# Kernel tuning notes

Measured on AMD Instinct MI355X. Metric: run time of the kernel, lower is better.

The kernel has to match this reference:

```python
import jax, jax.numpy as jnp
import numpy as np

B, S, D, L = 8, 512, 768, 200


def leaky(x, slope=0.2):
    return jnp.where(x >= 0, x, slope * x)


def l1_normalize(x, axis):
    # torch.nn.functional.normalize(p=1): x / max(sum|x|, 1e-12)
    return x / jnp.maximum(jnp.sum(jnp.abs(x), axis=axis, keepdims=True), 1e-12)


def setup_inputs() -> dict:
    key = jax.random.key(0)
    ks = jax.random.split(key, 16)
    s = 1.0 / np.sqrt(D)
    return {
        "doc_embedding": jax.random.normal(ks[0], (B, S, D), jnp.float32),
        "labels": jax.random.uniform(ks[1], (B, L), jnp.float32),
        "label_embed": jax.random.normal(ks[2], (L, D), jnp.float32),
        "label_adj": jax.random.uniform(ks[3], (L, L), jnp.float32),
        "w_gcn3": jax.random.uniform(ks[4], (D, D), jnp.float32, -s, s),
        "w_gcn5": jax.random.uniform(ks[5], (D, D), jnp.float32, -s, s),
        "w_ll1": jax.random.normal(ks[6], (D, D), jnp.float32) * s,
        "b_ll1": jax.random.normal(ks[7], (D,), jnp.float32) * s,
        "w_ll2": jax.random.normal(ks[8], (D, D), jnp.float32) * s,
        "b_ll2": jax.random.normal(ks[9], (D,), jnp.float32) * s,
        "w_lin": jax.random.normal(ks[10], (2 * D, D), jnp.float32) * (1.0 / np.sqrt(2 * D)),
        "b_lin": jax.random.normal(ks[11], (D,), jnp.float32) * s,
        "conv_w": jax.random.normal(ks[12], (L, 1, 9, 9), jnp.float32) * (1.0 / 9.0),
        "conv_b": jax.random.normal(ks[13], (L,), jnp.float32) * 0.01,
        "w_lin1": jax.random.normal(ks[14], (D, L), jnp.float32) * s,
        "b_lin1": jax.random.normal(ks[15], (L,), jnp.float32) * s,
    }


def reference(doc_embedding, labels, label_embed, label_adj, w_gcn3, w_gcn5,
              w_ll1, b_ll1, w_ll2, b_ll2, w_lin, b_lin, conv_w, conv_b,
              w_lin1, b_lin1):
    b = doc_embedding.shape[0]
    # stacked (replicated) label embeddings: [B, L, D]
    le = jnp.broadcast_to(label_embed, (b,) + label_embed.shape)

    # GCN3: adj @ (x @ W), leaky relu 0.2
    le = leaky(jnp.einsum('lm,bmd->bld', label_adj, le @ w_gcn3))

    # learned adjacency A = sigmoid(lin1(le) @ lin2(le)^T)   [B, L, L]
    q = le @ w_ll1 + b_ll1
    k = le @ w_ll2 + b_ll2
    A = jax.nn.sigmoid(jnp.einsum('bld,bmd->blm', q, k))

    # normalize_adj: D^{-1/2} with detached row sum; out = (A D)^T D
    row_sum = jax.lax.stop_gradient(jnp.sum(A, axis=1))  # [B, L]
    d_inv_sqrt = jnp.where(row_sum > 0, row_sum ** -0.5, 0.0)
    AD = A * d_inv_sqrt[:, None, :]                 # A @ diag(d)
    A_norm = jnp.swapaxes(AD, 1, 2) * d_inv_sqrt[:, None, :]

    # GCN5 with learned adj
    d_le = leaky(jnp.einsum('blm,bmd->bld', A_norm, le @ w_gcn5))

    le_cat = jnp.concatenate([le, d_le], axis=-1)   # [B, L, 2D]
    le_out = le_cat @ w_lin + b_lin                 # [B, L, D]

    le_out = l1_normalize(le_out, axis=-2)
    doc = l1_normalize(doc_embedding, axis=-2)

    # word-label attention map [B, S, L]
    wla = jnp.einsum('bsd,bld->bsl', doc, le_out)

    # conv2d 1 -> L channels, 9x9, pad 4 over [B, 1, S, L]
    att = jax.lax.conv_general_dilated(
        wla[:, None, :, :], conv_w, window_strides=(1, 1),
        padding=((4, 4), (4, 4)),
        dimension_numbers=('NCHW', 'OIHW', 'NCHW'))
    att = att + conv_b[None, :, None, None]         # [B, L, S, L]

    att = jnp.max(att, axis=1)                      # [B, S, L]
    att = jnp.max(att, axis=-1, keepdims=True)      # [B, S, 1]
    gate = jnp.tanh(att)

    h_enc = jnp.sum(gate * doc, axis=1)             # [B, D]
    label_output = jax.nn.sigmoid(h_enc @ w_lin1 + b_lin1)

    eps = 1e-7
    p = jnp.clip(label_output, eps, 1.0 - eps)
    loss = -jnp.mean(labels * jnp.log(p) + (1.0 - labels) * jnp.log(1.0 - p))
    return label_output, loss
```

## Files before the change

### kernel.cpp

```cpp
#include <hip/hip_runtime.h>
#include <hip/hip_bf16.h>
#include <math.h>

#define BB 8
#define SS 512
#define DD 768
#define LL 200

typedef __attribute__((ext_vector_type(8))) short bf16x8;
typedef __attribute__((ext_vector_type(4))) float f32x4;

__device__ inline short f2bf(float f) {
    unsigned u = __builtin_bit_cast(unsigned, f);
    unsigned r = (u + 0x7FFFu + ((u >> 16) & 1u)) >> 16;
    return (short)r;
}
__device__ inline float bf2f(short s) {
    unsigned u = ((unsigned)(unsigned short)s) << 16;
    return __builtin_bit_cast(float, u);
}

#define LDP3 264
#define BK3  256
#define MGLDS (2 * 64 * LDP3 * 2)

template<int EPI, bool TB>
__global__ __launch_bounds__(256, 1) void mgemm_k(
    const short* __restrict__ A, int lda,
    const void* __restrict__ Bv, int ldb,
    const float* __restrict__ bias,
    const void* __restrict__ Bv2, const float* __restrict__ bias2, int nsplit,
    const void* __restrict__ Bv3, const float* __restrict__ bias3, int nsplit2,
    float* __restrict__ Cf, int ldc,
    short* __restrict__ Cb, int ldcb,
    short* __restrict__ Ct, int ldct, int nsplitT,
    int M, int N, int K)
{
    extern __shared__ short dsm[];
    short* As = dsm;
    short* Bs = dsm + 64 * LDP3;
    const int tid = threadIdx.x;
    const int bm = blockIdx.y * 64;
    const int bn = blockIdx.x * 64;
    int bnb = bn;
    if (!TB) {
        if (bn >= nsplit2)      { Bv = Bv3; bias = bias3; bnb = bn - nsplit2; }
        else if (bn >= nsplit)  { Bv = Bv2; bias = bias2; bnb = bn - nsplit; }
    }
    const int w = tid >> 6, lane = tid & 63, g = lane >> 4, ln = lane & 15;
    const int Kp = (K + BK3 - 1) & ~(BK3 - 1);
    const int nt = Kp >> 8;

    const int ar = tid >> 2, ac = tid & 3;
    const int bn_ = tid & 63, bko = (tid >> 6) * 64;

    f32x4 acc[4];
    #pragma unroll
    for (int i = 0; i < 4; ++i) acc[i] = (f32x4){0.f, 0.f, 0.f, 0.f};

    bf16x8 aR[8], bT[8];
    #pragma unroll
    for (int j = 0; j < 8; ++j) { aR[j] = (bf16x8){0,0,0,0,0,0,0,0}; bT[j] = (bf16x8){0,0,0,0,0,0,0,0}; }
    float bF[64];
    #pragma unroll
    for (int j = 0; j < 64; ++j) bF[j] = 0.f;

    const int gmS = bm + ar;
    const bool aOk = (gmS < M);

    auto fetchA = [&](int k0) {
        if (aOk) {
            const short* p = A + (size_t)gmS * lda + k0 + ac * 64;
            #pragma unroll
            for (int j = 0; j < 8; ++j) aR[j] = *(const bf16x8*)(p + j * 8);
        }
    };
    auto fetchB = [&](int k0) {
        if (TB) {
            const short* Bt = (const short*)Bv;
            int gn = bn + ar;
            if (gn < N) {
                const short* p = Bt + (size_t)gn * ldb + k0 + ac * 64;
                #pragma unroll
                for (int j = 0; j < 8; ++j) bT[j] = *(const bf16x8*)(p + j * 8);
            }
        } else {
            const float* Bp = (const float*)Bv + (size_t)(bnb + bn_);
            #pragma unroll
            for (int j = 0; j < 64; ++j) {
                int gk = k0 + bko + j;
                bF[j] = (gk < K) ? Bp[(size_t)gk * ldb] : 0.f;
            }
        }
    };

    fetchA(0);
    fetchB(0);

    for (int t = 0; t < nt; ++t) {
        {
            short* pa = As + ar * LDP3 + ac * 64;
            #pragma unroll
            for (int j = 0; j < 8; ++j) *(bf16x8*)(pa + j * 8) = aR[j];
        }
        if (TB) {
            short* pb = Bs + ar * LDP3 + ac * 64;
            #pragma unroll
            for (int j = 0; j < 8; ++j) *(bf16x8*)(pb + j * 8) = bT[j];
        } else {
            short* pb = Bs + bn_ * LDP3 + bko;
            #pragma unroll
            for (int q = 0; q < 8; ++q) {
                bf16x8 v;
                #pragma unroll
                for (int e = 0; e < 8; ++e) v[e] = f2bf(bF[q * 8 + e]);
                *(bf16x8*)(pb + q * 8) = v;
            }
        }
        __syncthreads();

        if (t + 1 < nt) {
            int k0 = (t + 1) << 8;
            fetchA(k0);
            fetchB(k0);
        }

        #pragma unroll
        for (int ks = 0; ks < 8; ++ks) {
            bf16x8 a = *(const bf16x8*)(As + (w * 16 + ln) * LDP3 + ks * 32 + g * 8);
            #pragma unroll
            for (int nb = 0; nb < 4; ++nb) {
                bf16x8 b = *(const bf16x8*)(Bs + (nb * 16 + ln) * LDP3 + ks * 32 + g * 8);
                acc[nb] = __builtin_amdgcn_mfma_f32_16x16x32_bf16(a, b, acc[nb], 0, 0, 0);
            }
        }
        __syncthreads();
    }

    #pragma unroll
    for (int nb = 0; nb < 4; ++nb) {
        int gn = bn + nb * 16 + ln;
        float bv = (bias && gn < N) ? bias[bnb + nb * 16 + ln] : 0.f;
        #pragma unroll
        for (int r = 0; r < 4; ++r) {
            int gm = bm + w * 16 + g * 4 + r;
            if (gm < M && gn < N) {
                float v = acc[nb][r] + bv;
                if (EPI == 1) v = (v >= 0.f) ? v : 0.2f * v;
                else if (EPI == 2) v = 1.f / (1.f + expf(-v));
                if (Cf) Cf[(size_t)gm * ldc + gn] = v;
                if (Cb) Cb[(size_t)gm * ldcb + gn] = f2bf(v);
                if (Ct && gn >= nsplitT)
                    Ct[(size_t)(gn - nsplitT) * ldct + gm] = f2bf(v);
            }
        }
    }
}

#define WP 168
#define TP 24
#define WTR 217
#define WROWS 208
#define APAD 256
#define BIGN (1 << 30)

__global__ void prep_k(const float* __restrict__ cw, const float* __restrict__ cb,
                       const float* __restrict__ adj,
                       short* __restrict__ wkg, short* __restrict__ adj_bf)
{
    int idx = blockIdx.x * blockDim.x + threadIdx.x;
    if (idx < WROWS * WP) {
        int o = idx / WP, kk = idx % WP;
        int kj = kk >> 4, ki = kk & 15;
        float v = 0.f;
        if (o < LL && kj < 9) {
            if (ki < 9) v = cw[o * 81 + ki * 9 + kj];
            else if (ki == 9 && kj == 0) v = cb[o];
        }
        wkg[idx] = f2bf(v);
        return;
    }
    idx -= WROWS * WP;
    if (idx < LL * APAD) {
        int r = idx / APAD, c = idx % APAD;
        adj_bf[idx] = f2bf(c < LL ? adj[r * LL + c] : 0.f);
    }
}

__global__ void ca_k(const float* __restrict__ A, short* __restrict__ An)
{
    int i = blockIdx.x;
    int j = threadIdx.x;
    float si = 0.f, sj = 0.f;
    for (int l = 0; l < LL; ++l) {
        si += A[l * LL + i];
        if (j < LL) sj += A[l * LL + j];
    }
    float di = (si > 0.f) ? (1.f / sqrtf(si)) : 0.f;
    float dj = (sj > 0.f) ? (1.f / sqrtf(sj)) : 0.f;
    float v = (j < LL) ? A[j * LL + i] * di * dj : 0.f;
    An[i * APAD + j] = f2bf(v);
}

__global__ void l1n_k(const float* __restrict__ X, short* __restrict__ Xb)
{
    int c = threadIdx.x >> 5, r = threadIdx.x & 31;
    int col = blockIdx.x * 8 + c;
    float s = 0.f;
    for (int l = r; l < LL; l += 32) s += fabsf(X[l * DD + col]);
    #pragma unroll
    for (int off = 16; off > 0; off >>= 1) s += __shfl_xor(s, off, 64);
    float inv = 1.f / fmaxf(s, 1e-12f);
    for (int l = r; l < LL; l += 32)
        Xb[l * DD + col] = f2bf(X[l * DD + col] * inv);
}

__global__ void docsumA_k(const float* __restrict__ doc, float* __restrict__ dpart)
{
    int dc = blockIdx.x, sc = blockIdx.y, b = blockIdx.z;
    int dx = threadIdx.x & 63, sy = threadIdx.x >> 6;
    int d = dc * 64 + dx;
    const float* pp = doc + ((size_t)b * SS + sc * 64) * DD + d;
    float s = 0.f;
    for (int t = sy; t < 64; t += 4) s += fabsf(pp[(size_t)t * DD]);
    __shared__ float red[4][64];
    red[sy][dx] = s;
    __syncthreads();
    if (sy == 0)
        dpart[((size_t)b * 8 + sc) * DD + d] = red[0][dx] + red[1][dx] + red[2][dx] + red[3][dx];
}

__global__ void docbfB_k(const float* __restrict__ doc, const float* __restrict__ dpart,
                         short* __restrict__ docb)
{
    int gid = blockIdx.x * blockDim.x + threadIdx.x;
    if (gid >= BB * SS * DD / 4) return;
    size_t base = (size_t)gid * 4;
    int d = (int)(base % DD);
    int b = (int)(base / ((size_t)SS * DD));
    float4 v = *(const float4*)(doc + base);
    float4 dn = {0.f, 0.f, 0.f, 0.f};
    #pragma unroll
    for (int sc = 0; sc < 8; ++sc) {
        float4 t = *(const float4*)(dpart + ((size_t)b * 8 + sc) * DD + d);
        dn.x += t.x; dn.y += t.y; dn.z += t.z; dn.w += t.w;
    }
    dn.x = fmaxf(dn.x, 1e-12f); dn.y = fmaxf(dn.y, 1e-12f);
    dn.z = fmaxf(dn.z, 1e-12f); dn.w = fmaxf(dn.w, 1e-12f);
    short4 o;
    o.x = f2bf(v.x / dn.x);
    o.y = f2bf(v.y / dn.y);
    o.z = f2bf(v.z / dn.z);
    o.w = f2bf(v.w / dn.w);
    *(short4*)(docb + base) = o;
}

__global__ __launch_bounds__(512, 1) void conv_max_k(
    const float* __restrict__ wla,
    const short* __restrict__ wkg,
    float* __restrict__ gate)
{
    extern __shared__ short smem[];
    short* Wk   = smem;
    short* winT = Wk + WROWS * WP;
    short* wbf  = winT + 4 * WTR * TP;
    __shared__ float wredf[8];

    const int blk = blockIdx.x;
    const int b = blk >> 7;
    const int s0 = (blk & 127) << 2;
    const int tid = threadIdx.x;

    {
        const int4* src = (const int4*)wkg;
        int4* dst = (int4*)Wk;
        for (int i = tid; i < WROWS * WP / 8; i += 512) dst[i] = src[i];
    }
    for (int idx = tid; idx < 12 * 216; idx += 512) {
        int r = idx / 216, c = idx % 216;
        int sr = s0 - 4 + r, col = c - 4;
        float v = 0.f;
        if (sr >= 0 && sr < SS && col >= 0 && col < LL)
            v = wla[((size_t)b * SS + sr) * LL + col];
        wbf[idx] = f2bf(v);
    }
    __syncthreads();
    for (int idx = tid; idx < 4 * WTR; idx += 512) {
        int p = idx / WTR, r = idx % WTR;
        short vals[16];
        #pragma unroll
        for (int i = 0; i < 9; ++i) vals[i] = (r < 216) ? wbf[(p + i) * 216 + r] : (short)0;
        vals[9] = (short)0x3F80;
        #pragma unroll
        for (int i = 10; i < 16; ++i) vals[i] = 0;
        short* dstp = winT + (p * WTR + r) * TP;
        *(bf16x8*)dstp = *(const bf16x8*)vals;
        *(bf16x8*)(dstp + 8) = *(const bf16x8*)(vals + 8);
    }
    __syncthreads();

    const int w = tid >> 6;
    const int p = w >> 1;
    const int h = w & 1;
    const int lane = tid & 63;
    const int g = lane >> 4;
    const int ln = lane & 15;
    const short* WT = winT + p * WTR * TP;

    bf16x8 Af[7][5];
    #pragma unroll
    for (int s = 0; s < 7; ++s) {
        int st = h * 7 + s;
        if (st > 12) st = 12;
        #pragma unroll
        for (int j = 0; j < 5; ++j)
            Af[s][j] = *(const bf16x8*)(Wk + (st * 16 + ln) * WP + j * 32 + g * 8);
    }

    float lm = -INFINITY;

    auto loadB = [&](int nt, bf16x8 (&Bf)[5]) {
        #pragma unroll
        for (int j = 0; j < 5; ++j)
            Bf[j] = *(const bf16x8*)(WT + (nt * 16 + ln + 2 * j + (g >> 1)) * TP + (g & 1) * 8);
    };
    auto compute = [&](int nt, const bf16x8 (&Bf)[5]) {
        #pragma unroll
        for (int s = 0; s < 7; ++s) {
            if (h == 0 || s < 6) {
                int st = h * 7 + s;
                f32x4 acc = {0.f, 0.f, 0.f, 0.f};
                #pragma unroll
                for (int j = 0; j < 5; ++j)
                    acc = __builtin_amdgcn_mfma_f32_16x16x32_bf16(Af[s][j], Bf[j], acc, 0, 0, 0);
                float t = fmaxf(fmaxf(acc[0], acc[1]), fmaxf(acc[2], acc[3]));
                bool ok = (st < 12 || g < 2) && (nt < 12 || ln < 8);
                lm = ok ? fmaxf(lm, t) : lm;
            }
        }
    };

    bf16x8 B0[5], B1[5];
    loadB(0, B0);
    for (int nt = 0; nt < 12; nt += 2) {
        loadB(nt + 1, B1);
        compute(nt, B0);
        loadB(nt + 2, B0);
        compute(nt + 1, B1);
    }
    compute(12, B0);

    #pragma unroll
    for (int off = 32; off > 0; off >>= 1)
        lm = fmaxf(lm, __shfl_xor(lm, off, 64));
    if (lane == 0) wredf[w] = lm;
    __syncthreads();
    if (tid < 4)
        gate[((size_t)b << 9) + s0 + tid] = tanhf(fmaxf(wredf[2 * tid], wredf[2 * tid + 1]));
}

__global__ void henc_part_k(const short* __restrict__ doc_nb, const float* __restrict__ gate,
                            float* __restrict__ hpart)
{
    int dc = blockIdx.x, sc = blockIdx.y, b = blockIdx.z;
    int dx = threadIdx.x & 63, sy = threadIdx.x >> 6;
    int d = dc * 64 + dx;
    float s = 0.f;
    for (int t = sy; t < 64; t += 4) {
        int srow = sc * 64 + t;
        s = fmaf(bf2f(doc_nb[((size_t)b * SS + srow) * DD + d]), gate[b * SS + srow], s);
    }
    __shared__ float red[4][64];
    red[sy][dx] = s;
    __syncthreads();
    if (sy == 0)
        hpart[((size_t)b * 8 + sc) * DD + d] = red[0][dx] + red[1][dx] + red[2][dx] + red[3][dx];
}

__global__ void final2_k(const float* __restrict__ hpart,
                         const float* __restrict__ W, const float* __restrict__ bias,
                         float* __restrict__ out)
{
    int b = blockIdx.x, tid = threadIdx.x;
    __shared__ float hb[DD];
    for (int idx = tid; idx < DD; idx += 256) {
        float s = 0.f;
        #pragma unroll
        for (int sc = 0; sc < 8; ++sc) s += hpart[((size_t)b * 8 + sc) * DD + idx];
        hb[idx] = s;
    }
    __syncthreads();
    int l = tid;
    if (l < LL) {
        float acc = bias[l];
        for (int d = 0; d < DD; ++d) acc = fmaf(hb[d], W[d * LL + l], acc);
        out[b * LL + l] = 1.f / (1.f + expf(-acc));
    }
}

__global__ void loss_k(const float* __restrict__ out, const float* __restrict__ labels,
                       float* __restrict__ loss_out)
{
    float s = 0.f;
    for (int i = threadIdx.x; i < BB * LL; i += 256) {
        float p = out[i];
        p = fminf(fmaxf(p, 1e-7f), 1.f - 1e-7f);
        float y = labels[i];
        s += y * logf(p) + (1.f - y) * logf(1.f - p);
    }
    #pragma unroll
    for (int off = 32; off > 0; off >>= 1) s += __shfl_down(s, off, 64);
    __shared__ float ws[4];
    if ((threadIdx.x & 63) == 0) ws[threadIdx.x >> 6] = s;
    __syncthreads();
    if (threadIdx.x == 0)
        loss_out[0] = -(ws[0] + ws[1] + ws[2] + ws[3]) / (float)(BB * LL);
}

static void mgemm(hipStream_t st, int epi, bool tb,
                  const short* A, int lda, const void* B, int ldb,
                  const float* bias,
                  const void* B2, const float* bias2, int nsplit,
                  const void* B3, const float* bias3, int nsplit2,
                  float* Cf, int ldc, short* Cb, int ldcb,
                  short* Ct, int ldct, int nsplitT,
                  int M, int N, int K)
{
    dim3 g((N + 63) / 64, (M + 63) / 64);
    #define LAUNCH(E, T) do { \
        (void)hipFuncSetAttribute((const void*)mgemm_k<E, T>, \
                                  hipFuncAttributeMaxDynamicSharedMemorySize, MGLDS); \
        mgemm_k<E, T><<<g, 256, MGLDS, st>>>(A, lda, B, ldb, bias, B2, bias2, nsplit, \
                                             B3, bias3, nsplit2, Cf, ldc, Cb, ldcb, \
                                             Ct, ldct, nsplitT, M, N, K); \
    } while (0)
    if (!tb) {
        if (epi == 0)      LAUNCH(0, false);
        else if (epi == 1) LAUNCH(1, false);
        else               LAUNCH(2, false);
    } else {
        if (epi == 0)      LAUNCH(0, true);
        else if (epi == 1) LAUNCH(1, true);
        else               LAUNCH(2, true);
    }
    #undef LAUNCH
}

extern "C" void kernel_launch(void* const* d_in, const int* in_sizes, int n_in,
                              void* d_out, int out_size, void* d_ws, size_t ws_size,
                              hipStream_t stream)
{
    const float* doc_emb   = (const float*)d_in[0];
    const float* labels    = (const float*)d_in[1];
    const float* label_emb = (const float*)d_in[2];
    const float* label_adj = (const float*)d_in[3];
    const float* w_gcn3    = (const float*)d_in[4];
    const float* w_gcn5    = (const float*)d_in[5];
    const float* w_ll1     = (const float*)d_in[6];
    const float* b_ll1     = (const float*)d_in[7];
    const float* w_ll2     = (const float*)d_in[8];
    const float* b_ll2     = (const float*)d_in[9];
    const float* w_lin     = (const float*)d_in[10];
    const float* b_lin     = (const float*)d_in[11];
    const float* conv_w    = (const float*)d_in[12];
    const float* conv_b    = (const float*)d_in[13];
    const float* w_lin1    = (const float*)d_in[14];
    const float* b_lin1    = (const float*)d_in[15];

    float* out = (float*)d_out;

    char* p = (char*)d_ws;
    auto alloc = [&](size_t bytes) { void* r = p; p += (bytes + 15) & ~(size_t)15; return r; };
    short* wkg       = (short*)alloc(WROWS * WP * 2);
    short* adj_bf    = (short*)alloc(200 * APAD * 2);
    short* E2_bf     = (short*)alloc(200 * 768 * 2);
    short* le_cat_bf = (short*)alloc(200 * 1536 * 2);
    short* qkh_bf    = (short*)alloc(200 * 2304 * 2);
    short* Ht        = (short*)alloc(768 * 256 * 2);
    float* Amat      = (float*)alloc(200 * 200 * 4);
    short* Anorm_bf  = (short*)alloc(200 * APAD * 2);
    float* le_out_f  = (float*)alloc(200 * 768 * 4);
    short* le_out_bf = (short*)alloc(200 * 768 * 2);
    float* dpart     = (float*)alloc(BB * 8 * DD * 4);
    short* doc_nb    = (short*)alloc((size_t)BB * SS * DD * 2);
    float* wla       = (float*)alloc((size_t)BB * SS * LL * 4);
    float* gatev     = (float*)alloc(BB * SS * 4);
    float* hpart     = (float*)alloc(BB * 8 * DD * 4);

    docsumA_k<<<dim3(12, 8, 8), 256, 0, stream>>>(doc_emb, dpart);
    docbfB_k<<<(BB * SS * DD / 4 + 255) / 256, 256, 0, stream>>>(doc_emb, dpart, doc_nb);
    prep_k<<<(WROWS * WP + LL * APAD + 255) / 256, 256, 0, stream>>>(
        conv_w, conv_b, label_adj, wkg, adj_bf);
    mgemm(stream, 0, false, adj_bf, APAD, label_emb, DD, nullptr,
          nullptr, nullptr, BIGN, nullptr, nullptr, BIGN,
          nullptr, 0, E2_bf, DD, nullptr, 0, BIGN, LL, DD, LL);
    mgemm(stream, 1, false, E2_bf, DD, w_gcn3, DD, nullptr,
          nullptr, nullptr, BIGN, nullptr, nullptr, BIGN,
          nullptr, 0, le_cat_bf, 1536, nullptr, 0, BIGN, LL, DD, DD);
    mgemm(stream, 0, false, le_cat_bf, 1536, w_ll1, DD, b_ll1,
          w_ll2, b_ll2, DD, w_gcn5, nullptr, 2 * DD,
          nullptr, 0, qkh_bf, 2304, Ht, 256, 2 * DD, LL, 3 * DD, DD);
    mgemm(stream, 2, true, qkh_bf, 2304, qkh_bf + DD, 2304, nullptr,
          nullptr, nullptr, BIGN, nullptr, nullptr, BIGN,
          Amat, LL, nullptr, 0, nullptr, 0, BIGN, LL, LL, DD);
    ca_k<<<LL, 256, 0, stream>>>(Amat, Anorm_bf);
    mgemm(stream, 1, true, Anorm_bf, APAD, Ht, 256, nullptr,
          nullptr, nullptr, BIGN, nullptr, nullptr, BIGN,
          nullptr, 0, le_cat_bf + DD, 1536, nullptr, 0, BIGN, LL, DD, LL);
    mgemm(stream, 0, false, le_cat_bf, 1536, w_lin, DD, b_lin,
          nullptr, nullptr, BIGN, nullptr, nullptr, BIGN,
          le_out_f, DD, nullptr, 0, nullptr, 0, BIGN, LL, DD, 2 * DD);
    l1n_k<<<96, 256, 0, stream>>>(le_out_f, le_out_bf);
    mgemm(stream, 0, true, doc_nb, DD, le_out_bf, DD, nullptr,
          nullptr, nullptr, BIGN, nullptr, nullptr, BIGN,
          wla, LL, nullptr, 0, nullptr, 0, BIGN, BB * SS, LL, DD);
    (void)hipFuncSetAttribute((const void*)conv_max_k,
                              hipFuncAttributeMaxDynamicSharedMemorySize, 116736);
    conv_max_k<<<1024, 512, 116736, stream>>>(wla, wkg, gatev);
    henc_part_k<<<dim3(12, 8, 8), 256, 0, stream>>>(doc_nb, gatev, hpart);
    final2_k<<<BB, 256, 0, stream>>>(hpart, w_lin1, b_lin1, out);
    loss_k<<<1, 256, 0, stream>>>(out, labels, out + BB * LL);
}
```

Baseline: 277.4 us.

## Split conv-max over label-channel halves across blocks and defer tanh to henc

```diff
diff --git a/kernel.cpp b/kernel.cpp
--- a/kernel.cpp
+++ b/kernel.cpp
@@ -255,41 +255,87 @@
     *(short4*)(docb + base) = o;
 }
 
-__global__ __launch_bounds__(512, 1) void conv_max_k(
+template<int NS>
+__device__ __forceinline__ void conv_body2(const short* __restrict__ Wlh,
+                                           const short* __restrict__ WT,
+                                           int lrow0, int soffG,
+                                           int ln, int g, float& lm)
+{
+    bf16x8 Af[NS][5];
+    #pragma unroll
+    for (int s = 0; s < NS; ++s)
+        #pragma unroll
+        for (int j = 0; j < 5; ++j)
+            Af[s][j] = *(const bf16x8*)(Wlh + (lrow0 + s * 16 + ln) * WP + j * 32 + g * 8);
+
+    #pragma unroll 1
+    for (int nt = 0; nt < 13; ++nt) {
+        bf16x8 Bf[5];
+        #pragma unroll
+        for (int j = 0; j < 5; ++j)
+            Bf[j] = *(const bf16x8*)(WT + (nt * 16 + ln + 2 * j + (g >> 1)) * TP + (g & 1) * 8);
+
+        f32x4 acc[NS];
+        #pragma unroll
+        for (int s = 0; s < NS; ++s) acc[s] = (f32x4){0.f, 0.f, 0.f, 0.f};
+
+        #pragma unroll
+        for (int j = 0; j < 5; ++j)
+            #pragma unroll
+            for (int s = 0; s < NS; ++s)
+                acc[s] = __builtin_amdgcn_mfma_f32_16x16x32_bf16(Af[s][j], Bf[j], acc[s], 0, 0, 0);
+
+        bool colOK = (nt < 12) | (ln < 8);
+        #pragma unroll
+        for (int s = 0; s < NS; ++s) {
+            float t = fmaxf(fmaxf(acc[s][0], acc[s][1]), fmaxf(acc[s][2], acc[s][3]));
+            bool ok = colOK & ((soffG + s < 12) | (g < 2));
+            lm = ok ? fmaxf(lm, t) : lm;
+        }
+    }
+}
+
+__global__ __launch_bounds__(512, 2) void conv_max_k(
     const float* __restrict__ wla,
     const short* __restrict__ wkg,
-    float* __restrict__ gate)
+    float* __restrict__ ghalf)
 {
     extern __shared__ short smem[];
-    short* Wk   = smem;
-    short* winT = Wk + WROWS * WP;
-    short* wbf  = winT + 4 * WTR * TP;
+    short* Wlh  = smem;
+    short* winT = Wlh + 112 * WP;
     __shared__ float wredf[8];
 
     const int blk = blockIdx.x;
-    const int b = blk >> 7;
-    const int s0 = (blk & 127) << 2;
+    const int h = blk & 1;
+    const int sg = (blk >> 1) & 127;
+    const int b = blk >> 8;
+    const int s0 = sg << 2;
     const int tid = threadIdx.x;
 
     {
         const int4* src = (const int4*)wkg;
-        int4* dst = (int4*)Wk;
-        for (int i = tid; i < WROWS * WP / 8; i += 512) dst[i] = src[i];
-    }
-    for (int idx = tid; idx < 12 * 216; idx += 512) {
-        int r = idx / 216, c = idx % 216;
-        int sr = s0 - 4 + r, col = c - 4;
-        float v = 0.f;
-        if (sr >= 0 && sr < SS && col >= 0 && col < LL)
-            v = wla[((size_t)b * SS + sr) * LL + col];
-        wbf[idx] = f2bf(v);
-    }
-    __syncthreads();
+        int4* dst = (int4*)Wlh;
+        const int row0 = h * 112;
+        for (int i = tid; i < 112 * 21; i += 512) {
+            int r = i / 21, c = i % 21;
+            int gr = row0 + r;
+            int4 v = {0, 0, 0, 0};
+            if (gr < WROWS) v = src[gr * 21 + c];
+            dst[i] = v;
+        }
+    }
     for (int idx = tid; idx < 4 * WTR; idx += 512) {
         int p = idx / WTR, r = idx % WTR;
+        int col = r - 4;
         short vals[16];
         #pragma unroll
-        for (int i = 0; i < 9; ++i) vals[i] = (r < 216) ? wbf[(p + i) * 216 + r] : (short)0;
+        for (int i = 0; i < 9; ++i) {
+            int srow = s0 + p - 4 + i;
+            float v = 0.f;
+            if (srow >= 0 && srow < SS && col >= 0 && col < LL)
+                v = wla[((size_t)b * SS + srow) * LL + col];
+            vals[i] = f2bf(v);
+        }
         vals[9] = (short)0x3F80;
         #pragma unroll
         for (int i = 10; i < 16; ++i) vals[i] = 0;
@@ -301,54 +347,20 @@
 
     const int w = tid >> 6;
     const int p = w >> 1;
-    const int h = w & 1;
+    const int q = w & 1;
     const int lane = tid & 63;
     const int g = lane >> 4;
     const int ln = lane & 15;
     const short* WT = winT + p * WTR * TP;
 
-    bf16x8 Af[7][5];
-    #pragma unroll
-    for (int s = 0; s < 7; ++s) {
-        int st = h * 7 + s;
-        if (st > 12) st = 12;
-        #pragma unroll
-        for (int j = 0; j < 5; ++j)
-            Af[s][j] = *(const bf16x8*)(Wk + (st * 16 + ln) * WP + j * 32 + g * 8);
-    }
-
     float lm = -INFINITY;
-
-    auto loadB = [&](int nt, bf16x8 (&Bf)[5]) {
-        #pragma unroll
-        for (int j = 0; j < 5; ++j)
-            Bf[j] = *(const bf16x8*)(WT + (nt * 16 + ln + 2 * j + (g >> 1)) * TP + (g & 1) * 8);
-    };
-    auto compute = [&](int nt, const bf16x8 (&Bf)[5]) {
-        #pragma unroll
-        for (int s = 0; s < 7; ++s) {
-            if (h == 0 || s < 6) {
-                int st = h * 7 + s;
-                f32x4 acc = {0.f, 0.f, 0.f, 0.f};
-                #pragma unroll
-                for (int j = 0; j < 5; ++j)
-                    acc = __builtin_amdgcn_mfma_f32_16x16x32_bf16(Af[s][j], Bf[j], acc, 0, 0, 0);
-                float t = fmaxf(fmaxf(acc[0], acc[1]), fmaxf(acc[2], acc[3]));
-                bool ok = (st < 12 || g < 2) && (nt < 12 || ln < 8);
-                lm = ok ? fmaxf(lm, t) : lm;
-            }
-        }
-    };
-
-    bf16x8 B0[5], B1[5];
-    loadB(0, B0);
-    for (int nt = 0; nt < 12; nt += 2) {
-        loadB(nt + 1, B1);
-        compute(nt, B0);
-        loadB(nt + 2, B0);
-        compute(nt + 1, B1);
-    }
-    compute(12, B0);
+    if (h == 0) {
+        if (q == 0) conv_body2<4>(Wlh, WT, 0,  0,  ln, g, lm);
+        else        conv_body2<3>(Wlh, WT, 64, 4,  ln, g, lm);
+    } else {
+        if (q == 0) conv_body2<3>(Wlh, WT, 0,  7,  ln, g, lm);
+        else        conv_body2<3>(Wlh, WT, 48, 10, ln, g, lm);
+    }
 
     #pragma unroll
     for (int off = 32; off > 0; off >>= 1)
@@ -356,21 +368,29 @@
     if (lane == 0) wredf[w] = lm;
     __syncthreads();
     if (tid < 4)
-        gate[((size_t)b << 9) + s0 + tid] = tanhf(fmaxf(wredf[2 * tid], wredf[2 * tid + 1]));
-}
-
-__global__ void henc_part_k(const short* __restrict__ doc_nb, const float* __restrict__ gate,
+        ghalf[(size_t)h * (BB * SS) + ((size_t)b << 9) + s0 + tid] =
+            fmaxf(wredf[2 * tid], wredf[2 * tid + 1]);
+}
+
+__global__ void henc_part_k(const short* __restrict__ doc_nb, const float* __restrict__ ghalf,
                             float* __restrict__ hpart)
 {
     int dc = blockIdx.x, sc = blockIdx.y, b = blockIdx.z;
     int dx = threadIdx.x & 63, sy = threadIdx.x >> 6;
     int d = dc * 64 + dx;
+    __shared__ float gsh[64];
+    __shared__ float red[4][64];
+    if (threadIdx.x < 64) {
+        int srow = sc * 64 + threadIdx.x;
+        size_t bs = (size_t)b * SS + srow;
+        gsh[threadIdx.x] = tanhf(fmaxf(ghalf[bs], ghalf[(size_t)BB * SS + bs]));
+    }
+    __syncthreads();
     float s = 0.f;
     for (int t = sy; t < 64; t += 4) {
         int srow = sc * 64 + t;
-        s = fmaf(bf2f(doc_nb[((size_t)b * SS + srow) * DD + d]), gate[b * SS + srow], s);
-    }
-    __shared__ float red[4][64];
+        s = fmaf(bf2f(doc_nb[((size_t)b * SS + srow) * DD + d]), gsh[t], s);
+    }
     red[sy][dx] = s;
     __syncthreads();
     if (sy == 0)
@@ -484,7 +504,7 @@
     float* dpart     = (float*)alloc(BB * 8 * DD * 4);
     short* doc_nb    = (short*)alloc((size_t)BB * SS * DD * 2);
     float* wla       = (float*)alloc((size_t)BB * SS * LL * 4);
-    float* gatev     = (float*)alloc(BB * SS * 4);
+    float* ghalf     = (float*)alloc(2 * BB * SS * 4);
     float* hpart     = (float*)alloc(BB * 8 * DD * 4);
 
     docsumA_k<<<dim3(12, 8, 8), 256, 0, stream>>>(doc_emb, dpart);
@@ -515,9 +535,9 @@
           nullptr, nullptr, BIGN, nullptr, nullptr, BIGN,
           wla, LL, nullptr, 0, nullptr, 0, BIGN, BB * SS, LL, DD);
     (void)hipFuncSetAttribute((const void*)conv_max_k,
-                              hipFuncAttributeMaxDynamicSharedMemorySize, 116736);
-    conv_max_k<<<1024, 512, 116736, stream>>>(wla, wkg, gatev);
-    henc_part_k<<<dim3(12, 8, 8), 256, 0, stream>>>(doc_nb, gatev, hpart);
+                              hipFuncAttributeMaxDynamicSharedMemorySize, 79296);
+    conv_max_k<<<2048, 512, 79296, stream>>>(wla, wkg, ghalf);
+    henc_part_k<<<dim3(12, 8, 8), 256, 0, stream>>>(doc_nb, ghalf, hpart);
     final2_k<<<BB, 256, 0, stream>>>(hpart, w_lin1, b_lin1, out);
     loss_k<<<1, 256, 0, stream>>>(out, labels, out + BB * LL);
 }
```

Result: faster. 270.8 us (-2.4%).
